# Kernel optimization log

Hardware: AMD Instinct MI355X
Metric: run time of the kernel (lower is better)

The kernel has to match this reference:

```python
import jax, jax.numpy as jnp
import numpy as np

NUM_HEADS = 12

def setup_inputs() -> dict:
    key = jax.random.key(0)
    ks = jax.random.split(key, 8)
    B, N, C = 8, 1024, 768
    H = NUM_HEADS
    return {
        "x": jax.random.normal(ks[0], (B, N, C), dtype=jnp.float32),
        "relative_position_index": jax.random.randint(ks[1], (N, N), 0, 2048, dtype=jnp.int64),
        "qkv_weight": jax.random.normal(ks[2], (3 * C, C), dtype=jnp.float32) * 0.02,
        "q_bias": jax.random.normal(ks[3], (C,), dtype=jnp.float32) * 0.02,
        "v_bias": jax.random.normal(ks[4], (C,), dtype=jnp.float32) * 0.02,
        "proj_weight": jax.random.normal(ks[5], (C, C), dtype=jnp.float32) * 0.02,
        "proj_bias": jax.random.normal(ks[6], (C,), dtype=jnp.float32) * 0.02,
        "rel_pos_bias_table": jax.random.normal(ks[7], (2048, H), dtype=jnp.float32) * 0.02,
    }

def reference(x, relative_position_index, qkv_weight, q_bias, v_bias, proj_weight, proj_bias, rel_pos_bias_table):
    B, N, C = x.shape
    H = NUM_HEADS
    d = C // H
    scale = d ** (-0.5)
    # qkv bias: (q_bias, zeros, v_bias) as in the torch module
    qkv_b = jnp.concatenate([q_bias, jnp.zeros_like(v_bias), v_bias])
    qkv = x @ qkv_weight.T + qkv_b  # [B,N,3C]
    qkv = qkv.reshape(B, N, 3, H, d).transpose(2, 0, 3, 1, 4)  # [3,B,H,N,d]
    q, k, v = qkv[0], qkv[1], qkv[2]
    attn = jnp.einsum("bhnd,bhmd->bhnm", q * scale, k)  # [B,H,N,N]
    # relative position bias: table lookup [N,N,H] -> [H,N,N]
    bias = rel_pos_bias_table[relative_position_index].transpose(2, 0, 1)
    attn = attn + bias[None]
    attn = jax.nn.softmax(attn, axis=-1)
    out = jnp.einsum("bhnm,bhmd->bhnd", attn, v)  # [B,H,N,d]
    out = out.transpose(0, 2, 1, 3).reshape(B, N, C)
    return out @ proj_weight.T + proj_bias
```

## Files before the change

kernel.cpp:

```cpp
#include <hip/hip_runtime.h>

typedef unsigned short ushort_t;
typedef __bf16 bf16x8 __attribute__((ext_vector_type(8)));
typedef float f32x4 __attribute__((ext_vector_type(4)));
typedef unsigned int u32x4 __attribute__((ext_vector_type(4)));

#define MFMA(a, b, c) __builtin_amdgcn_mfma_f32_16x16x32_bf16((a), (b), (c), 0, 0, 0)

#define BATCH 8
#define SEQ 1024
#define CDIM 768
#define NH 12
#define HD 64
#define MTOT (BATCH * SEQ)
#define THREEC (3 * CDIM)
#define KVB 64
#define LOG2E 1.44269504088896f

__device__ __forceinline__ ushort_t f2bf(float f) {
    unsigned int u = __builtin_bit_cast(unsigned int, f);
    u = (u + 0x7FFFu + ((u >> 16) & 1u)) >> 16;
    return (ushort_t)u;
}
__device__ __forceinline__ float bf2f(ushort_t b) {
    unsigned int u = ((unsigned int)b) << 16;
    return __builtin_bit_cast(float, u);
}
__device__ __forceinline__ ushort_t bfbits(float f) {
    __bf16 h = (__bf16)f;
    return __builtin_bit_cast(ushort_t, h);
}
__device__ __forceinline__ unsigned int pack2bf(float a, float b) {
    ushort2 p;
    p.x = bfbits(a);
    p.y = bfbits(b);
    return __builtin_bit_cast(unsigned int, p);
}

typedef const __attribute__((address_space(1))) unsigned int* gas_ptr;
typedef __attribute__((address_space(3))) unsigned int* las_ptr;

__device__ __forceinline__ void async16(const ushort_t* g, ushort_t* l) {
    __builtin_amdgcn_global_load_lds((gas_ptr)(const void*)g, (las_ptr)(void*)l, 16, 0, 0);
}

#define WAITVM_(N) asm volatile("s_waitcnt vmcnt(" #N ")" ::: "memory")
#define WAITVM(N) WAITVM_(N)
#define SCHEDB __builtin_amdgcn_sched_barrier(0)

__global__ __launch_bounds__(256) void k_convert(const float* __restrict__ x,
                                                 const float* __restrict__ wq,
                                                 const float* __restrict__ wp,
                                                 ushort_t* __restrict__ xb,
                                                 ushort_t* __restrict__ wqb,
                                                 ushort_t* __restrict__ wpb) {
    const int NX = MTOT * CDIM / 4;
    const int NQ = THREEC * CDIM / 4;
    const int NP = CDIM * CDIM / 4;
    int i = blockIdx.x * 256 + threadIdx.x;
    const float4* src;
    ushort_t* dst;
    int off;
    if (i < NX) { src = (const float4*)x; dst = xb; off = i; }
    else if (i < NX + NQ) { src = (const float4*)wq; dst = wqb; off = i - NX; }
    else if (i < NX + NQ + NP) { src = (const float4*)wp; dst = wpb; off = i - NX - NQ; }
    else return;
    float4 v = src[off];
    ushort4 o;
    o.x = f2bf(v.x); o.y = f2bf(v.y); o.z = f2bf(v.z); o.w = f2bf(v.w);
    ((ushort4*)dst)[off] = o;
}

__global__ __launch_bounds__(256) void k_bias(const int* __restrict__ rpi,
                                              const float* __restrict__ table,
                                              ushort_t* __restrict__ biasF) {
    __shared__ int idx_s[16][64];
    int tr = blockIdx.x;
    int tcq = blockIdx.y;
    int t = threadIdx.x;
    {
        int r = t >> 4;
        int c4 = (t & 15) * 4;
        int4 v = *(const int4*)&rpi[(tr * 16 + r) * SEQ + tcq * 64 + c4];
        *(int4*)&idx_s[r][c4] = v;
    }
    __syncthreads();
    int j = t >> 6;
    int lane = t & 63;
    int lq = lane >> 4, l15 = lane & 15;
    int tc = tcq * 4 + j;
    int id[4];
#pragma unroll
    for (int rr = 0; rr < 4; rr++) id[rr] = idx_s[l15][j * 16 + lq * 4 + rr];
#pragma unroll
    for (int h = 0; h < NH; h++) {
        ushort4 o;
        o.x = f2bf(table[id[0] * NH + h] * LOG2E);
        o.y = f2bf(table[id[1] * NH + h] * LOG2E);
        o.z = f2bf(table[id[2] * NH + h] * LOG2E);
        o.w = f2bf(table[id[3] * NH + h] * LOG2E);
        *(ushort4*)&biasF[(((h * 64 + tr) * 64 + tc) * 256 + lane * 4)] = o;
    }
}

template <int MODE>
__global__ __launch_bounds__(256) void k_gemm(const ushort_t* __restrict__ A,
                                              const ushort_t* __restrict__ Bw,
                                              const float* __restrict__ biasq,
                                              const float* __restrict__ biasv,
                                              const float* __restrict__ biasp,
                                              ushort_t* __restrict__ qb,
                                              ushort_t* __restrict__ kb,
                                              ushort_t* __restrict__ vT,
                                              float* __restrict__ outp) {
    __shared__ __attribute__((aligned(16))) ushort_t As[128 * 64];
    __shared__ __attribute__((aligned(16))) ushort_t Bs[128 * 64];
    const int K = CDIM;
    int tid = threadIdx.x, wave = tid >> 6, lane = tid & 63;
    int l15 = lane & 15, lq = lane >> 4;
    int wm = wave >> 1, wn = wave & 1;
    int rowBase = blockIdx.y * 128;
    int colBase = blockIdx.x * 128;
    f32x4 acc[4][4] = {};
    int srow = wave * 8 + (lane >> 3);
    int scol = (((lane & 7) ^ (srow & 7))) * 8;
    int l7 = l15 & 7;
    for (int k0 = 0; k0 < K; k0 += 64) {
#pragma unroll
        for (int is = 0; is < 4; is++) {
            async16(A + (rowBase + is * 32 + srow) * K + k0 + scol,
                    As + is * 2048 + tid * 8);
            async16(Bw + (colBase + is * 32 + srow) * K + k0 + scol,
                    Bs + is * 2048 + tid * 8);
        }
        asm volatile("s_waitcnt vmcnt(0)" ::: "memory");
        __syncthreads();
#pragma unroll
        for (int kk = 0; kk < 64; kk += 32) {
            bf16x8 af[4], bfr[4];
#pragma unroll
            for (int mf = 0; mf < 4; mf++)
                af[mf] = *(const bf16x8*)&As[(wm * 64 + mf * 16 + l15) * 64 +
                                             ((((kk >> 3) + lq) ^ l7) * 8)];
#pragma unroll
            for (int nf = 0; nf < 4; nf++)
                bfr[nf] = *(const bf16x8*)&Bs[(wn * 64 + nf * 16 + l15) * 64 +
                                              ((((kk >> 3) + lq) ^ l7) * 8)];
#pragma unroll
            for (int mf = 0; mf < 4; mf++)
#pragma unroll
                for (int nf = 0; nf < 4; nf++)
                    acc[mf][nf] = MFMA(af[mf], bfr[nf], acc[mf][nf]);
        }
        __syncthreads();
    }
#pragma unroll
    for (int mf = 0; mf < 4; mf++) {
#pragma unroll
        for (int nf = 0; nf < 4; nf++) {
            int jc = colBase + wn * 64 + nf * 16 + l15;
            int mg0 = rowBase + wm * 64 + mf * 16 + (lane >> 4) * 4;
            if (MODE == 0) {
                int which = jc / CDIM;
                int co = jc - which * CDIM;
                int b = mg0 >> 10, tok0 = mg0 & 1023;
                int hh = co >> 6, dd = co & 63;
                int bh = b * NH + hh;
                if (which == 0) {
                    float bq_ = biasq[co];
#pragma unroll
                    for (int r = 0; r < 4; r++)
                        qb[(bh * SEQ + tok0 + r) * HD + dd] =
                            f2bf((acc[mf][nf][r] + bq_) * 0.125f);
                } else if (which == 1) {
#pragma unroll
                    for (int r = 0; r < 4; r++)
                        kb[(bh * SEQ + tok0 + r) * HD + dd] = f2bf(acc[mf][nf][r]);
                } else {
                    float bv = biasv[co];
                    ushort4 pk;
                    pk.x = f2bf(acc[mf][nf][0] + bv);
                    pk.y = f2bf(acc[mf][nf][1] + bv);
                    pk.z = f2bf(acc[mf][nf][2] + bv);
                    pk.w = f2bf(acc[mf][nf][3] + bv);
                    *(ushort4*)&vT[(size_t)(bh * HD + dd) * SEQ + tok0] = pk;
                }
            } else {
                float bp_ = biasp[jc];
#pragma unroll
                for (int r = 0; r < 4; r++)
                    outp[(size_t)(mg0 + r) * CDIM + jc] = acc[mf][nf][r] + bp_;
            }
        }
    }
}

__global__ __launch_bounds__(256, 4) void k_attn(const ushort_t* __restrict__ qb,
                                                 const ushort_t* __restrict__ kb,
                                                 const ushort_t* __restrict__ vT,
                                                 const ushort_t* __restrict__ biasF,
                                                 ushort_t* __restrict__ ctx) {
    __shared__ __attribute__((aligned(16))) ushort_t Ks[2][KVB * 64];
    __shared__ __attribute__((aligned(16))) ushort_t Vs[KVB * 64];

    int lin = ((int)blockIdx.x & 7) * 192 + ((int)blockIdx.x >> 3);
    int h = lin >> 7;
    int b = (lin >> 4) & 7;
    int qt = lin & 15;
    int bh = b * NH + h;
    int tid = threadIdx.x, w = tid >> 6, lane = tid & 63;
    int l15 = lane & 15, lq = lane >> 4, lq4 = lq * 4;
    int row0 = qt * 64 + w * 16;
    int qtile0 = row0 >> 4;

    const ushort_t* qp = qb + bh * SEQ * HD;
    const ushort_t* kp = kb + bh * SEQ * HD;
    const ushort_t* vp = vT + bh * HD * SEQ;
    const ushort_t* bfp = biasF + (size_t)(h * 64 + qtile0) * 64 * 256;

    int lamA = l15 + 32 * (lq & 1);
    int lamB = lamA + 16;

    int rk0, sk0, rk1, sk1;
    {
        int cid0 = tid;
        rk0 = cid0 >> 3; sk0 = ((cid0 & 7) ^ (rk0 & 7)) * 8;
        int cid1 = 256 + tid;
        rk1 = cid1 >> 3; sk1 = ((cid1 & 7) ^ (rk1 & 7)) * 8;
    }

#define STAGE_K(BUF, C0)                                                    \
    do {                                                                    \
        async16(kp + ((C0) + rk0) * HD + sk0, &Ks[BUF][tid * 8]);           \
        async16(kp + ((C0) + rk1) * HD + sk1, &Ks[BUF][(256 + tid) * 8]);   \
    } while (0)
#define STAGE_V(C0)                                                         \
    do {                                                                    \
        async16(vp + rk0 * SEQ + (C0) + sk0, &Vs[tid * 8]);                 \
        async16(vp + rk1 * SEQ + (C0) + sk1, &Vs[(256 + tid) * 8]);         \
    } while (0)

    STAGE_K(0, 0); STAGE_V(0); STAGE_K(1, KVB);

    bf16x8 qfr0 = *(const bf16x8*)&qp[(row0 + l15) * HD + 8 * lq];
    bf16x8 qfr1 = *(const bf16x8*)&qp[(row0 + l15) * HD + 32 + 8 * lq];

    f32x4 Oa[4] = {};
    float mi = -1e30f, li = 0.0f;
    f32x4 accA[4], accB[4];
    unsigned int u0[4][2];

#define QK_BLOCK(AN, KN)                                                       \
    do {                                                                       \
        __builtin_amdgcn_s_setprio(1);                                         \
        _Pragma("unroll") for (int n = 0; n < 4; n++) {                        \
            int krow = n * 16 + l15;                                           \
            bf16x8 kf0 = *(const bf16x8*)&(KN)[krow * 64 + ((lq ^ (krow & 7)) * 8)]; \
            bf16x8 kf1 = *(const bf16x8*)&(KN)[krow * 64 + (((lq + 4) ^ (krow & 7)) * 8)]; \
            f32x4 z0 = {};                                                     \
            z0 = MFMA(kf0, qfr0, z0); z0 = MFMA(kf1, qfr1, z0);                \
            (AN)[n] = z0;                                                      \
        }                                                                      \
        __builtin_amdgcn_s_setprio(0);                                         \
    } while (0)

#define SOFTMAX_STEP(ACC, BFR)                                                 \
    do {                                                                       \
        f32x4 z[4];                                                            \
        _Pragma("unroll") for (int n = 0; n < 4; n++) {                        \
            z[n][0] = fmaf((ACC)[n][0], LOG2E, bf2f((BFR)[n].x));              \
            z[n][1] = fmaf((ACC)[n][1], LOG2E, bf2f((BFR)[n].y));              \
            z[n][2] = fmaf((ACC)[n][2], LOG2E, bf2f((BFR)[n].z));              \
            z[n][3] = fmaf((ACC)[n][3], LOG2E, bf2f((BFR)[n].w));              \
        }                                                                      \
        float tm;                                                              \
        {                                                                      \
            f32x4 mv;                                                          \
            _Pragma("unroll") for (int j = 0; j < 4; j++)                      \
                mv[j] = fmaxf(fmaxf(z[0][j], z[1][j]), fmaxf(z[2][j], z[3][j])); \
            tm = fmaxf(fmaxf(mv[0], mv[1]), fmaxf(mv[2], mv[3]));              \
        }                                                                      \
        tm = fmaxf(tm, __shfl_xor(tm, 16));                                    \
        tm = fmaxf(tm, __shfl_xor(tm, 32));                                    \
        if (!__all(tm <= mi + 8.0f)) {                                         \
            float mn = fmaxf(mi, tm);                                          \
            float al = exp2f(mi - mn);                                         \
            mi = mn; li *= al;                                                 \
            _Pragma("unroll") for (int r = 0; r < 4; r++) {                    \
                float alr = __shfl(al, (lane & 48) | (lq4 + r));               \
                Oa[0][r] *= alr; Oa[1][r] *= alr;                              \
                Oa[2][r] *= alr; Oa[3][r] *= alr;                              \
            }                                                                  \
        }                                                                      \
        f32x4 sv = {};                                                         \
        _Pragma("unroll") for (int n = 0; n < 4; n++) {                        \
            z[n][0] = exp2f(z[n][0] - mi); z[n][1] = exp2f(z[n][1] - mi);      \
            z[n][2] = exp2f(z[n][2] - mi); z[n][3] = exp2f(z[n][3] - mi);      \
            sv += z[n];                                                        \
        }                                                                      \
        float s = (sv[0] + sv[1]) + (sv[2] + sv[3]);                           \
        s += __shfl_xor(s, 16);                                                \
        s += __shfl_xor(s, 32);                                                \
        li += s;                                                               \
        _Pragma("unroll") for (int n = 0; n < 4; n++) {                        \
            u0[n][0] = pack2bf(z[n][0], z[n][1]);                              \
            u0[n][1] = pack2bf(z[n][2], z[n][3]);                              \
        }                                                                      \
    } while (0)

#define ASSEMBLE(KS, PF)                                                       \
    do {                                                                       \
        unsigned int a0 = __shfl((int)u0[2 * (KS)][0], lamA);                  \
        unsigned int b0 = __shfl((int)u0[2 * (KS) + 1][0], lamA);              \
        unsigned int a1 = __shfl((int)u0[2 * (KS)][1], lamA);                  \
        unsigned int b1 = __shfl((int)u0[2 * (KS) + 1][1], lamA);              \
        unsigned int a2 = __shfl((int)u0[2 * (KS)][0], lamB);                  \
        unsigned int b2 = __shfl((int)u0[2 * (KS) + 1][0], lamB);              \
        unsigned int a3 = __shfl((int)u0[2 * (KS)][1], lamB);                  \
        unsigned int b3 = __shfl((int)u0[2 * (KS) + 1][1], lamB);              \
        bool hi_ = (lq & 2) != 0;                                              \
        u32x4 qd;                                                              \
        qd[0] = hi_ ? b0 : a0; qd[1] = hi_ ? b1 : a1;                          \
        qd[2] = hi_ ? b2 : a2; qd[3] = hi_ ? b3 : a3;                          \
        (PF) = __builtin_bit_cast(bf16x8, qd);                                 \
    } while (0)

#define PV_BLOCK()                                                             \
    do {                                                                       \
        __builtin_amdgcn_s_setprio(1);                                         \
        _Pragma("unroll") for (int ks = 0; ks < 2; ks++) {                     \
            bf16x8 pfa;                                                        \
            ASSEMBLE(ks, pfa);                                                 \
            _Pragma("unroll") for (int nc = 0; nc < 4; nc++) {                 \
                int vrow = nc * 16 + l15;                                      \
                bf16x8 vf = *(const bf16x8*)&Vs[vrow * 64 + (((ks * 4 + lq) ^ (vrow & 7)) * 8)]; \
                Oa[nc] = MFMA(pfa, vf, Oa[nc]);                                \
            }                                                                  \
        }                                                                      \
        __builtin_amdgcn_s_setprio(0);                                         \
    } while (0)

#define ITER(T, AC, AN, DO_KST, DO_VST, DO_QK)                                 \
    do {                                                                       \
        WAITVM(0);                                                             \
        SCHEDB;                                                                \
        __builtin_amdgcn_s_barrier();                                          \
        SCHEDB;                                                                \
        const int t_ = (T);                                                    \
        ushort4 bfr0[4];                                                       \
        {                                                                      \
            int kt0 = t_ * 4;                                                  \
            _Pragma("unroll") for (int n = 0; n < 4; n++)                      \
                bfr0[n] = *(const ushort4*)&bfp[(kt0 + n) * 256 + lane * 4];   \
        }                                                                      \
        if (DO_KST) STAGE_K(t_ & 1, (t_ + 2) * KVB);                           \
        if (DO_QK) QK_BLOCK(AN, Ks[(t_ + 1) & 1]);                             \
        SOFTMAX_STEP(AC, bfr0);                                                \
        PV_BLOCK();                                                            \
        if (DO_VST) {                                                          \
            SCHEDB;                                                            \
            __builtin_amdgcn_s_barrier();                                      \
            SCHEDB;                                                            \
            STAGE_V((t_ + 1) * KVB);                                           \
        }                                                                      \
    } while (0)

    WAITVM(2);
    SCHEDB;
    __builtin_amdgcn_s_barrier();
    SCHEDB;
    QK_BLOCK(accA, Ks[0]);

#pragma unroll 1
    for (int tt = 0; tt < 14; tt += 2) {
        ITER(tt,     accA, accB, 1, 1, 1);
        ITER(tt + 1, accB, accA, 1, 1, 1);
    }
    ITER(14, accA, accB, 0, 1, 1);
    ITER(15, accB, accA, 0, 0, 0);

    float rli = 1.0f / li;
#pragma unroll
    for (int r = 0; r < 4; r++) {
        float rl = __shfl(rli, (lane & 48) | (lq4 + r));
#pragma unroll
        for (int nc = 0; nc < 4; nc++) {
            ctx[(size_t)(b * SEQ + row0 + lq4 + r) * CDIM + h * HD + nc * 16 + l15] =
                bfbits(Oa[nc][r] * rl);
        }
    }
#undef ITER
#undef PV_BLOCK
#undef ASSEMBLE
#undef SOFTMAX_STEP
#undef QK_BLOCK
#undef STAGE_V
#undef STAGE_K
}

extern "C" void kernel_launch(void* const* d_in, const int* in_sizes, int n_in,
                              void* d_out, int out_size, void* d_ws, size_t ws_size,
                              hipStream_t stream) {
    const float* x = (const float*)d_in[0];
    const int* rpi = (const int*)d_in[1];
    const float* wqkv = (const float*)d_in[2];
    const float* qbias = (const float*)d_in[3];
    const float* vbias = (const float*)d_in[4];
    const float* wproj = (const float*)d_in[5];
    const float* pbias = (const float*)d_in[6];
    const float* table = (const float*)d_in[7];
    float* out = (float*)d_out;

    char* ws = (char*)d_ws;
    ushort_t* xb    = (ushort_t*)(ws + 0);
    ushort_t* wqb   = (ushort_t*)(ws + 12582912);
    ushort_t* wpb   = (ushort_t*)(ws + 16121856);
    ushort_t* qbuf  = (ushort_t*)(ws + 17301504);
    ushort_t* kbuf  = (ushort_t*)(ws + 29884416);
    ushort_t* vTbuf = (ushort_t*)(ws + 42467328);
    ushort_t* ctx   = (ushort_t*)(ws + 55050240);
    ushort_t* biasF = (ushort_t*)(ws + 67633152);

    k_convert<<<8448, 256, 0, stream>>>(x, wqkv, wproj, xb, wqb, wpb);
    k_bias<<<dim3(64, 16), 256, 0, stream>>>(rpi, table, biasF);
    k_gemm<0><<<dim3(THREEC / 128, MTOT / 128), 256, 0, stream>>>(
        xb, wqb, qbias, vbias, nullptr, qbuf, kbuf, vTbuf, nullptr);
    k_attn<<<1536, 256, 0, stream>>>(qbuf, kbuf, vTbuf, biasF, ctx);
    k_gemm<1><<<dim3(CDIM / 128, MTOT / 128), 256, 0, stream>>>(
        ctx, wpb, nullptr, nullptr, pbias, nullptr, nullptr, nullptr, out);
}
```

Baseline: 170.0 us.

## Double KV tile to 128 rows and restructure attention pipeline waits

```diff
diff --git a/kernel.cpp b/kernel.cpp
--- a/kernel.cpp
+++ b/kernel.cpp
@@ -14,7 +14,7 @@
 #define HD 64
 #define MTOT (BATCH * SEQ)
 #define THREEC (3 * CDIM)
-#define KVB 64
+#define KVB 128
 #define LOG2E 1.44269504088896f
 
 __device__ __forceinline__ ushort_t f2bf(float f) {
@@ -195,13 +195,13 @@
     }
 }
 
-__global__ __launch_bounds__(256, 4) void k_attn(const ushort_t* __restrict__ qb,
+__global__ __launch_bounds__(256, 3) void k_attn(const ushort_t* __restrict__ qb,
                                                  const ushort_t* __restrict__ kb,
                                                  const ushort_t* __restrict__ vT,
                                                  const ushort_t* __restrict__ biasF,
                                                  ushort_t* __restrict__ ctx) {
     __shared__ __attribute__((aligned(16))) ushort_t Ks[2][KVB * 64];
-    __shared__ __attribute__((aligned(16))) ushort_t Vs[KVB * 64];
+    __shared__ __attribute__((aligned(16))) ushort_t Vs[64 * KVB];
 
     int lin = ((int)blockIdx.x & 7) * 192 + ((int)blockIdx.x >> 3);
     int h = lin >> 7;
@@ -221,39 +221,52 @@
     int lamA = l15 + 32 * (lq & 1);
     int lamB = lamA + 16;
 
-    int rk0, sk0, rk1, sk1;
-    {
-        int cid0 = tid;
-        rk0 = cid0 >> 3; sk0 = ((cid0 & 7) ^ (rk0 & 7)) * 8;
-        int cid1 = 256 + tid;
-        rk1 = cid1 >> 3; sk1 = ((cid1 & 7) ^ (rk1 & 7)) * 8;
-    }
-
-#define STAGE_K(BUF, C0)                                                    \
-    do {                                                                    \
-        async16(kp + ((C0) + rk0) * HD + sk0, &Ks[BUF][tid * 8]);           \
-        async16(kp + ((C0) + rk1) * HD + sk1, &Ks[BUF][(256 + tid) * 8]);   \
-    } while (0)
-#define STAGE_V(C0)                                                         \
-    do {                                                                    \
-        async16(vp + rk0 * SEQ + (C0) + sk0, &Vs[tid * 8]);                 \
-        async16(vp + rk1 * SEQ + (C0) + sk1, &Vs[(256 + tid) * 8]);         \
-    } while (0)
-
-    STAGE_K(0, 0); STAGE_V(0); STAGE_K(1, KVB);
+    int rkK[4], skK[4], rkV[4], skV[4];
+#pragma unroll
+    for (int j = 0; j < 4; j++) {
+        int cid = j * 256 + tid;
+        rkK[j] = cid >> 3;  skK[j] = ((cid & 7) ^ (rkK[j] & 7)) * 8;
+        rkV[j] = cid >> 4;  skV[j] = ((cid & 15) ^ (rkV[j] & 7)) * 8;
+    }
+
+#define STAGE_K(BUF, C0)                                                       \
+    do {                                                                       \
+        _Pragma("unroll") for (int j = 0; j < 4; j++)                          \
+            async16(kp + ((C0) + rkK[j]) * HD + skK[j],                        \
+                    &Ks[BUF][(j * 256 + tid) * 8]);                            \
+    } while (0)
+#define STAGE_V(C0)                                                            \
+    do {                                                                       \
+        _Pragma("unroll") for (int j = 0; j < 4; j++)                          \
+            async16(vp + rkV[j] * SEQ + (C0) + skV[j],                         \
+                    &Vs[(j * 256 + tid) * 8]);                                 \
+    } while (0)
+
+    ushort4 bfr[8];
+#define LOAD_BIAS(T)                                                           \
+    do {                                                                       \
+        int kt0 = (T) * 8;                                                     \
+        _Pragma("unroll") for (int n = 0; n < 8; n++)                          \
+            bfr[n] = *(const ushort4*)&bfp[(kt0 + n) * 256 + lane * 4];        \
+    } while (0)
 
     bf16x8 qfr0 = *(const bf16x8*)&qp[(row0 + l15) * HD + 8 * lq];
     bf16x8 qfr1 = *(const bf16x8*)&qp[(row0 + l15) * HD + 32 + 8 * lq];
 
+    STAGE_K(0, 0);
+    STAGE_K(1, KVB);
+    LOAD_BIAS(0);
+    STAGE_V(0);
+
     f32x4 Oa[4] = {};
     float mi = -1e30f, li = 0.0f;
-    f32x4 accA[4], accB[4];
-    unsigned int u0[4][2];
+    f32x4 accA[8], accB[8];
+    unsigned int u0[8][2];
 
 #define QK_BLOCK(AN, KN)                                                       \
     do {                                                                       \
         __builtin_amdgcn_s_setprio(1);                                         \
-        _Pragma("unroll") for (int n = 0; n < 4; n++) {                        \
+        _Pragma("unroll") for (int n = 0; n < 8; n++) {                        \
             int krow = n * 16 + l15;                                           \
             bf16x8 kf0 = *(const bf16x8*)&(KN)[krow * 64 + ((lq ^ (krow & 7)) * 8)]; \
             bf16x8 kf1 = *(const bf16x8*)&(KN)[krow * 64 + (((lq + 4) ^ (krow & 7)) * 8)]; \
@@ -264,21 +277,25 @@
         __builtin_amdgcn_s_setprio(0);                                         \
     } while (0)
 
-#define SOFTMAX_STEP(ACC, BFR)                                                 \
-    do {                                                                       \
-        f32x4 z[4];                                                            \
-        _Pragma("unroll") for (int n = 0; n < 4; n++) {                        \
-            z[n][0] = fmaf((ACC)[n][0], LOG2E, bf2f((BFR)[n].x));              \
-            z[n][1] = fmaf((ACC)[n][1], LOG2E, bf2f((BFR)[n].y));              \
-            z[n][2] = fmaf((ACC)[n][2], LOG2E, bf2f((BFR)[n].z));              \
-            z[n][3] = fmaf((ACC)[n][3], LOG2E, bf2f((BFR)[n].w));              \
+#define SOFTMAX_STEP(ACC)                                                      \
+    do {                                                                       \
+        _Pragma("unroll") for (int n = 0; n < 8; n++) {                        \
+            (ACC)[n][0] = fmaf((ACC)[n][0], LOG2E, bf2f(bfr[n].x));            \
+            (ACC)[n][1] = fmaf((ACC)[n][1], LOG2E, bf2f(bfr[n].y));            \
+            (ACC)[n][2] = fmaf((ACC)[n][2], LOG2E, bf2f(bfr[n].z));            \
+            (ACC)[n][3] = fmaf((ACC)[n][3], LOG2E, bf2f(bfr[n].w));            \
         }                                                                      \
         float tm;                                                              \
         {                                                                      \
-            f32x4 mv;                                                          \
-            _Pragma("unroll") for (int j = 0; j < 4; j++)                      \
-                mv[j] = fmaxf(fmaxf(z[0][j], z[1][j]), fmaxf(z[2][j], z[3][j])); \
-            tm = fmaxf(fmaxf(mv[0], mv[1]), fmaxf(mv[2], mv[3]));              \
+            f32x4 mv0, mv1;                                                    \
+            _Pragma("unroll") for (int j = 0; j < 4; j++) {                    \
+                mv0[j] = fmaxf(fmaxf((ACC)[0][j], (ACC)[1][j]),                \
+                               fmaxf((ACC)[2][j], (ACC)[3][j]));               \
+                mv1[j] = fmaxf(fmaxf((ACC)[4][j], (ACC)[5][j]),                \
+                               fmaxf((ACC)[6][j], (ACC)[7][j]));               \
+                mv0[j] = fmaxf(mv0[j], mv1[j]);                                \
+            }                                                                  \
+            tm = fmaxf(fmaxf(mv0[0], mv0[1]), fmaxf(mv0[2], mv0[3]));          \
         }                                                                      \
         tm = fmaxf(tm, __shfl_xor(tm, 16));                                    \
         tm = fmaxf(tm, __shfl_xor(tm, 32));                                    \
@@ -293,18 +310,20 @@
             }                                                                  \
         }                                                                      \
         f32x4 sv = {};                                                         \
-        _Pragma("unroll") for (int n = 0; n < 4; n++) {                        \
-            z[n][0] = exp2f(z[n][0] - mi); z[n][1] = exp2f(z[n][1] - mi);      \
-            z[n][2] = exp2f(z[n][2] - mi); z[n][3] = exp2f(z[n][3] - mi);      \
-            sv += z[n];                                                        \
+        _Pragma("unroll") for (int n = 0; n < 8; n++) {                        \
+            (ACC)[n][0] = exp2f((ACC)[n][0] - mi);                             \
+            (ACC)[n][1] = exp2f((ACC)[n][1] - mi);                             \
+            (ACC)[n][2] = exp2f((ACC)[n][2] - mi);                             \
+            (ACC)[n][3] = exp2f((ACC)[n][3] - mi);                             \
+            sv += (ACC)[n];                                                    \
         }                                                                      \
         float s = (sv[0] + sv[1]) + (sv[2] + sv[3]);                           \
         s += __shfl_xor(s, 16);                                                \
         s += __shfl_xor(s, 32);                                                \
         li += s;                                                               \
-        _Pragma("unroll") for (int n = 0; n < 4; n++) {                        \
-            u0[n][0] = pack2bf(z[n][0], z[n][1]);                              \
-            u0[n][1] = pack2bf(z[n][2], z[n][3]);                              \
+        _Pragma("unroll") for (int n = 0; n < 8; n++) {                        \
+            u0[n][0] = pack2bf((ACC)[n][0], (ACC)[n][1]);                      \
+            u0[n][1] = pack2bf((ACC)[n][2], (ACC)[n][3]);                      \
         }                                                                      \
     } while (0)
 
@@ -328,56 +347,57 @@
 #define PV_BLOCK()                                                             \
     do {                                                                       \
         __builtin_amdgcn_s_setprio(1);                                         \
-        _Pragma("unroll") for (int ks = 0; ks < 2; ks++) {                     \
+        _Pragma("unroll") for (int ks = 0; ks < 4; ks++) {                     \
             bf16x8 pfa;                                                        \
             ASSEMBLE(ks, pfa);                                                 \
             _Pragma("unroll") for (int nc = 0; nc < 4; nc++) {                 \
                 int vrow = nc * 16 + l15;                                      \
-                bf16x8 vf = *(const bf16x8*)&Vs[vrow * 64 + (((ks * 4 + lq) ^ (vrow & 7)) * 8)]; \
+                bf16x8 vf = *(const bf16x8*)&Vs[vrow * KVB +                   \
+                                                (((ks * 4 + lq) ^ (vrow & 7)) * 8)]; \
                 Oa[nc] = MFMA(pfa, vf, Oa[nc]);                                \
             }                                                                  \
         }                                                                      \
         __builtin_amdgcn_s_setprio(0);                                         \
     } while (0)
 
-#define ITER(T, AC, AN, DO_KST, DO_VST, DO_QK)                                 \
-    do {                                                                       \
-        WAITVM(0);                                                             \
+#define ITER(T, AC, AN, DO_KST, DO_VST, DO_QK, VMMID)                          \
+    do {                                                                       \
+        WAITVM(12);                         \
         SCHEDB;                                                                \
         __builtin_amdgcn_s_barrier();                                          \
         SCHEDB;                                                                \
         const int t_ = (T);                                                    \
-        ushort4 bfr0[4];                                                       \
-        {                                                                      \
-            int kt0 = t_ * 4;                                                  \
-            _Pragma("unroll") for (int n = 0; n < 4; n++)                      \
-                bfr0[n] = *(const ushort4*)&bfp[(kt0 + n) * 256 + lane * 4];   \
-        }                                                                      \
         if (DO_KST) STAGE_K(t_ & 1, (t_ + 2) * KVB);                           \
         if (DO_QK) QK_BLOCK(AN, Ks[(t_ + 1) & 1]);                             \
-        SOFTMAX_STEP(AC, bfr0);                                                \
+        SOFTMAX_STEP(AC);                       \
+        WAITVM(VMMID);                          \
+        SCHEDB;                                                                \
+        __builtin_amdgcn_s_barrier();                                          \
+        SCHEDB;                                                                \
         PV_BLOCK();                                                            \
+        SCHEDB;                                                                \
+        __builtin_amdgcn_s_barrier();                   \
+        SCHEDB;                                                                \
         if (DO_VST) {                                                          \
-            SCHEDB;                                                            \
-            __builtin_amdgcn_s_barrier();                                      \
-            SCHEDB;                                                            \
+            LOAD_BIAS(t_ + 1);                                                 \
             STAGE_V((t_ + 1) * KVB);                                           \
         }                                                                      \
     } while (0)
 
-    WAITVM(2);
+    WAITVM(16);
     SCHEDB;
     __builtin_amdgcn_s_barrier();
     SCHEDB;
     QK_BLOCK(accA, Ks[0]);
 
-#pragma unroll 1
-    for (int tt = 0; tt < 14; tt += 2) {
-        ITER(tt,     accA, accB, 1, 1, 1);
-        ITER(tt + 1, accB, accA, 1, 1, 1);
-    }
-    ITER(14, accA, accB, 0, 1, 1);
-    ITER(15, accB, accA, 0, 0, 0);
+    ITER(0, accA, accB, 1, 1, 1, 4);
+    ITER(1, accB, accA, 1, 1, 1, 4);
+    ITER(2, accA, accB, 1, 1, 1, 4);
+    ITER(3, accB, accA, 1, 1, 1, 4);
+    ITER(4, accA, accB, 1, 1, 1, 4);
+    ITER(5, accB, accA, 1, 1, 1, 4);
+    ITER(6, accA, accB, 0, 1, 1, 0);
+    ITER(7, accB, accA, 0, 0, 0, 0);
 
     float rli = 1.0f / li;
 #pragma unroll
@@ -394,6 +414,7 @@
 #undef ASSEMBLE
 #undef SOFTMAX_STEP
 #undef QK_BLOCK
+#undef LOAD_BIAS
 #undef STAGE_V
 #undef STAGE_K
 }
```

Result: slower. 173.6 us (+2.1%).
